# Optimization experiments

Measured on AMD Instinct MI355X. Metric: run time of the kernel, lower is better.

The kernel has to match this reference:

```python
import jax, jax.numpy as jnp
import numpy as np

N_NODES = 100000
BN_EPS = 1e-5


def gcn_conv(x, edge_index, W, b):
    # x: [N, Fin] -> [N, Fout]; symmetric-normalized aggregation with self-loops,
    # matching torch_geometric GCNConv defaults.
    n = x.shape[0]
    row, col = edge_index[0], edge_index[1]  # messages flow row -> col
    h = x @ W  # [N, Fout]
    deg = jnp.zeros((n,), dtype=h.dtype).at[col].add(1.0) + 1.0  # +1 for self-loop
    dinv = jax.lax.rsqrt(deg)  # deg >= 1 always
    norm = dinv[row] * dinv[col]  # [E]
    agg = jax.ops.segment_sum(h[row] * norm[:, None], col, num_segments=n)
    agg = agg + h * (dinv * dinv)[:, None]  # self-loop term, norm = 1/deg
    return agg + b


def batch_norm(x, gamma, beta):
    # BatchNorm1d in training mode: biased batch statistics over nodes.
    mean = jnp.mean(x, axis=0)
    var = jnp.mean((x - mean) ** 2, axis=0)
    return gamma * (x - mean) * jax.lax.rsqrt(var + BN_EPS) + beta


def setup_inputs() -> dict:
    key = jax.random.key(0)
    k = jax.random.split(key, 8)
    net_size1, hidden, net_size2 = 64, 128, 128
    x = jax.random.normal(k[0], (N_NODES, net_size1), dtype=jnp.float32)
    edge_index = jax.random.randint(k[1], (2, 1600000), 0, N_NODES, dtype=jnp.int64)
    s1 = 1.0 / np.sqrt(net_size1)
    s2 = 1.0 / np.sqrt(hidden)
    W1 = jax.random.normal(k[2], (net_size1, hidden), dtype=jnp.float32) * s1
    b1 = jnp.zeros((hidden,), dtype=jnp.float32)
    gamma = jnp.ones((hidden,), dtype=jnp.float32)
    beta = jnp.zeros((hidden,), dtype=jnp.float32)
    W2 = jax.random.normal(k[3], (hidden, net_size2), dtype=jnp.float32) * s2
    b2 = jnp.zeros((net_size2,), dtype=jnp.float32)
    return {"x": x, "edge_index": edge_index, "W1": W1, "b1": b1,
            "gamma": gamma, "beta": beta, "W2": W2, "b2": b2}


def reference(x, edge_index, W1, b1, gamma, beta, W2, b2):
    h = jax.nn.relu(gcn_conv(x, edge_index, W1, b1))
    h = batch_norm(h, gamma, beta)
    h = jax.nn.relu(gcn_conv(h, edge_index, W2, b2))
    return h
```

## Files before the change

kernel.cpp:

```cpp
#include <hip/hip_runtime.h>

#define BSZ_LG 9
#define BSZ 512

__device__ __forceinline__ float bf_lo(unsigned u) { return __uint_as_float(u << 16); }
__device__ __forceinline__ float bf_hi(unsigned u) { return __uint_as_float(u & 0xffff0000u); }
__device__ __forceinline__ float bf1(unsigned short s) { return __uint_as_float(((unsigned)s) << 16); }
__device__ __forceinline__ unsigned short f2bf(float f) {
    unsigned u = __float_as_uint(f);
    u += 0x7fffu + ((u >> 16) & 1u);
    return (unsigned short)(u >> 16);
}
__device__ __forceinline__ unsigned pack2(float a, float b) {
    return (unsigned)f2bf(a) | ((unsigned)f2bf(b) << 16);
}

__global__ void k_flags(const unsigned* __restrict__ x, const int* __restrict__ ei,
                        int* __restrict__ flagf, int* __restrict__ flage,
                        int* __restrict__ bcnt, int* __restrict__ stats) {
    int t = threadIdx.x;
    if (blockIdx.x == 0) {
        int c = 0;
        for (int i = t; i < 1024; i += 256) {
            unsigned e = (x[i] >> 23) & 0xffu;
            if (e >= 96u && e < 160u) c++;
        }
        __shared__ int s;
        if (t == 0) s = 0;
        __syncthreads();
        atomicAdd(&s, c);
        __syncthreads();
        if (t == 0) *flagf = (s > 512) ? 1 : 0;
    } else if (blockIdx.x == 1) {
        int nz = 0;
        for (int i = t; i < 2048; i += 256) nz |= ei[2 * i + 1];
        __shared__ int s2;
        if (t == 0) s2 = 0;
        __syncthreads();
        if (nz) atomicOr(&s2, 1);
        __syncthreads();
        if (t == 0) *flage = (s2 == 0) ? 1 : 0;
    } else if (blockIdx.x == 2) {
        bcnt[t] = 0;
    } else {
        stats[t] = 0;
    }
}

struct Cvt6 {
    const void* src[6];
    unsigned short* dst[6];
    int off[7];
};
__global__ void k_cvt6(Cvt6 a, const int* __restrict__ flagf) {
    int i = blockIdx.x * 256 + threadIdx.x;
    if (i >= a.off[6]) return;
    int s = 0;
#pragma unroll
    for (int j = 1; j < 6; ++j) if (i >= a.off[j]) s = j;
    int k = i - a.off[s];
    unsigned short v;
    if (*flagf) v = f2bf(((const float*)a.src[s])[k]);
    else        v = ((const unsigned short*)a.src[s])[k];
    a.dst[s][k] = v;
}

__global__ __launch_bounds__(256) void k_prep(
        const void* __restrict__ x, const float* __restrict__ dinv,
        const int* __restrict__ flagf, unsigned* __restrict__ xs32, int Nq) {
    int i = blockIdx.x * 256 + threadIdx.x;
    if (i >= Nq) return;
    int n = i >> 4;
    float di = dinv[n];
    float v0, v1, v2, v3;
    if (*flagf) {
        float4 f = ((const float4*)x)[i];
        v0 = f.x; v1 = f.y; v2 = f.z; v3 = f.w;
    } else {
        uint2 u = ((const uint2*)x)[i];
        v0 = bf_lo(u.x); v1 = bf_hi(u.x); v2 = bf_lo(u.y); v3 = bf_hi(u.y);
    }
    uint2 o; o.x = pack2(di * v0, di * v1); o.y = pack2(di * v2, di * v3);
    ((uint2*)xs32)[i] = o;
}

__global__ __launch_bounds__(256) void k_binA(
        const int* __restrict__ ei, const int* __restrict__ flage,
        int* __restrict__ bcnt, int E, int N, int NBUCK) {
    __shared__ int hist[256];
    int t = threadIdx.x;
    hist[t] = 0;
    __syncthreads();
    int st = *flage + 1;
    int base = blockIdx.x * 4096 + t;
#pragma unroll
    for (int i = 0; i < 16; ++i) {
        int e = base + i * 256;
        if (e < E) {
            int r = ei[(size_t)st * e];
            int c = ei[(size_t)st * (E + e)];
            if ((unsigned)r < (unsigned)N && (unsigned)c < (unsigned)N)
                atomicAdd(&hist[c >> BSZ_LG], 1);
        }
    }
    __syncthreads();
    if (t < NBUCK && hist[t] > 0) atomicAdd(&bcnt[t], hist[t]);
}

__global__ void k_bscan(const int* __restrict__ bcnt, int* __restrict__ bofs,
                        int* __restrict__ bcur, int NBUCK) {
    __shared__ int tmp[256];
    int t = threadIdx.x;
    int v = (t < NBUCK) ? bcnt[t] : 0;
    tmp[t] = v; __syncthreads();
    for (int off = 1; off < 256; off <<= 1) {
        int xv = (t >= off) ? tmp[t - off] : 0;
        __syncthreads();
        tmp[t] += xv;
        __syncthreads();
    }
    if (t < NBUCK) {
        int ex = tmp[t] - v;
        bofs[t] = ex;
        bcur[t] = ex;
        if (t == NBUCK - 1) bofs[NBUCK] = tmp[t];
    }
}

__global__ __launch_bounds__(256) void k_binB(
        const int* __restrict__ ei, const int* __restrict__ flage,
        int* __restrict__ bcur, unsigned* __restrict__ bins, int E, int N, int NBUCK) {
    __shared__ int hist[256], hincl[256], hofs[256], loc[256], gbase[256];
    __shared__ unsigned stage[4096];
    __shared__ unsigned char bseg[4096];
    int t = threadIdx.x;
    hist[t] = 0; loc[t] = 0;
    __syncthreads();
    int st = *flage + 1;
    int base = blockIdx.x * 4096 + t;
    int bs[16]; unsigned vs[16];
#pragma unroll
    for (int i = 0; i < 16; ++i) {
        int e = base + i * 256;
        bs[i] = -1; vs[i] = 0;
        if (e < E) {
            int r = ei[(size_t)st * e];
            int c = ei[(size_t)st * (E + e)];
            if ((unsigned)r < (unsigned)N && (unsigned)c < (unsigned)N) {
                bs[i] = c >> BSZ_LG;
                vs[i] = ((unsigned)r << BSZ_LG) | (unsigned)(c & (BSZ - 1));
                atomicAdd(&hist[bs[i]], 1);
            }
        }
    }
    __syncthreads();
    hincl[t] = hist[t];
    __syncthreads();
    for (int off = 1; off < 256; off <<= 1) {
        int xv = (t >= off) ? hincl[t - off] : 0;
        __syncthreads();
        hincl[t] += xv;
        __syncthreads();
    }
    hofs[t] = hincl[t] - hist[t];
    if (t < NBUCK && hist[t] > 0) gbase[t] = atomicAdd(&bcur[t], hist[t]);
    __syncthreads();
#pragma unroll
    for (int i = 0; i < 16; ++i) {
        if (bs[i] >= 0) {
            int l = atomicAdd(&loc[bs[i]], 1);
            int pos = hofs[bs[i]] + l;
            stage[pos] = vs[i];
            bseg[pos] = (unsigned char)bs[i];
        }
    }
    __syncthreads();
    int total = hincl[255];
    for (int j = t; j < total; j += 256) {
        int b = bseg[j];
        bins[gbase[b] + (j - hofs[b])] = stage[j];
    }
}

__global__ __launch_bounds__(512) void k_csr(
        const unsigned* __restrict__ bins, const int* __restrict__ bofs,
        int* __restrict__ csr, int* __restrict__ ofs, int* __restrict__ endv,
        float* __restrict__ dinv, int N) {
    __shared__ int tmp[BSZ];
    __shared__ int cur[BSZ];
    int b = blockIdx.x, t = threadIdx.x;
    int eb = bofs[b], ee = bofs[b + 1];
    tmp[t] = 0;
    __syncthreads();
    for (int p = eb + t; p < ee; p += BSZ)
        atomicAdd(&tmp[bins[p] & (BSZ - 1)], 1);
    __syncthreads();
    int v = tmp[t];
    for (int off = 1; off < BSZ; off <<= 1) {
        int xv = (t >= off) ? tmp[t - off] : 0;
        __syncthreads();
        tmp[t] += xv;
        __syncthreads();
    }
    int incl = tmp[t];
    int excl = incl - v;
    cur[t] = excl;
    int node = b * BSZ + t;
    if (node < N) {
        ofs[node]  = eb + excl;
        endv[node] = eb + incl;
        dinv[node] = rsqrtf((float)(v + 1));
    }
    __syncthreads();
    for (int p = eb + t; p < ee; p += BSZ) {
        unsigned x = bins[p];
        int cl = x & (BSZ - 1);
        int l = atomicAdd(&cur[cl], 1);
        csr[eb + l] = (int)(x >> BSZ_LG);
    }
}

__global__ __launch_bounds__(256) void k_agg1(
        const unsigned* __restrict__ xs32, const int* __restrict__ csr,
        const int* __restrict__ ofs, const int* __restrict__ endv,
        const float* __restrict__ dinv, unsigned* __restrict__ s1_32, int N) {
    int sub = threadIdx.x >> 5, lane = threadIdx.x & 31;
    int node = blockIdx.x * 8 + sub;
    if (node >= N) return;
    int beg = ofs[node], end = endv[node];
    unsigned self = xs32[(size_t)node * 32 + lane];
    float a0 = bf_lo(self), a1 = bf_hi(self);
    int p = beg;
    for (; p + 7 < end; p += 8) {
        int r0 = csr[p], r1 = csr[p+1], r2 = csr[p+2], r3 = csr[p+3];
        int r4 = csr[p+4], r5 = csr[p+5], r6 = csr[p+6], r7 = csr[p+7];
        unsigned u0 = xs32[(size_t)r0 * 32 + lane];
        unsigned u1 = xs32[(size_t)r1 * 32 + lane];
        unsigned u2 = xs32[(size_t)r2 * 32 + lane];
        unsigned u3 = xs32[(size_t)r3 * 32 + lane];
        unsigned u4 = xs32[(size_t)r4 * 32 + lane];
        unsigned u5 = xs32[(size_t)r5 * 32 + lane];
        unsigned u6 = xs32[(size_t)r6 * 32 + lane];
        unsigned u7 = xs32[(size_t)r7 * 32 + lane];
        a0 += bf_lo(u0) + bf_lo(u1) + bf_lo(u2) + bf_lo(u3)
            + bf_lo(u4) + bf_lo(u5) + bf_lo(u6) + bf_lo(u7);
        a1 += bf_hi(u0) + bf_hi(u1) + bf_hi(u2) + bf_hi(u3)
            + bf_hi(u4) + bf_hi(u5) + bf_hi(u6) + bf_hi(u7);
    }
    for (; p + 3 < end; p += 4) {
        int r0 = csr[p], r1 = csr[p+1], r2 = csr[p+2], r3 = csr[p+3];
        unsigned u0 = xs32[(size_t)r0 * 32 + lane];
        unsigned u1 = xs32[(size_t)r1 * 32 + lane];
        unsigned u2 = xs32[(size_t)r2 * 32 + lane];
        unsigned u3 = xs32[(size_t)r3 * 32 + lane];
        a0 += bf_lo(u0) + bf_lo(u1) + bf_lo(u2) + bf_lo(u3);
        a1 += bf_hi(u0) + bf_hi(u1) + bf_hi(u2) + bf_hi(u3);
    }
    for (; p < end; ++p) {
        unsigned u = xs32[(size_t)csr[p] * 32 + lane];
        a0 += bf_lo(u); a1 += bf_hi(u);
    }
    float di = dinv[node];
    s1_32[(size_t)node * 32 + lane] = pack2(di * a0, di * a1);
}

typedef __attribute__((ext_vector_type(8))) short bf16x8;
typedef __attribute__((ext_vector_type(4))) float f32x4;

template<int K, int OUTMODE>
__global__ __launch_bounds__(256) void k_mgemm(
        const unsigned short* __restrict__ A, const unsigned short* __restrict__ Wg,
        const unsigned short* __restrict__ bias, void* __restrict__ outv,
        const int* __restrict__ flagf, int N) {
    constexpr int KP = K + 8;
    __shared__ __align__(16) unsigned short sA[64 * KP];
    __shared__ __align__(16) unsigned short sW[128 * KP];
    int t = threadIdx.x;
    int n0 = blockIdx.x * 64;

    for (int i = t; i < K * 128; i += 256) {
        int k = i >> 7, n = i & 127;
        sW[n * KP + k] = Wg[i];
    }
    {
        constexpr int rowv = K / 8;
        const uint4* Av = (const uint4*)A;
        for (int i = t; i < 64 * rowv; i += 256) {
            int r = i / rowv, c = i % rowv;
            int node = n0 + r;
            uint4 v = make_uint4(0u, 0u, 0u, 0u);
            if (node < N) v = Av[(size_t)node * rowv + c];
            *(uint4*)&sA[r * KP + c * 8] = v;
        }
    }
    __syncthreads();

    int lane = t & 63, wave = t >> 6, quad = lane >> 4, l16 = lane & 15;
    int mb = wave * 16;

    f32x4 acc[8];
#pragma unroll
    for (int j = 0; j < 8; ++j) acc[j] = (f32x4){0.f, 0.f, 0.f, 0.f};

#pragma unroll
    for (int k0 = 0; k0 < K; k0 += 32) {
        bf16x8 af = *(const bf16x8*)&sA[(mb + l16) * KP + k0 + quad * 8];
#pragma unroll
        for (int tn = 0; tn < 8; ++tn) {
            bf16x8 bfv = *(const bf16x8*)&sW[(tn * 16 + l16) * KP + k0 + quad * 8];
            acc[tn] = __builtin_amdgcn_mfma_f32_16x16x32_bf16(af, bfv, acc[tn], 0, 0, 0);
        }
    }

    bool f32out = (OUTMODE == 1) && (*flagf != 0);
    int nodeb = n0 + mb + quad * 4;
#pragma unroll
    for (int tn = 0; tn < 8; ++tn) {
        float bv = bf1(bias[tn * 16 + l16]);
#pragma unroll
        for (int r = 0; r < 4; ++r) {
            int node = nodeb + r;
            if (node < N) {
                float v = fmaxf(acc[tn][r] + bv, 0.f);
                if (OUTMODE == 1 && f32out)
                    ((float*)outv)[(size_t)node * 128 + tn * 16 + l16] = v;
                else
                    ((unsigned short*)outv)[(size_t)node * 128 + tn * 16 + l16] = f2bf(v);
            }
        }
    }
}

__global__ __launch_bounds__(256) void k_bnstat(
        const unsigned short* __restrict__ h1, float* __restrict__ stats, int N) {
    __shared__ float sS[1024], sQ[1024];
    int t = threadIdx.x;
    int lane = t & 31, g = t >> 5;
    int f0 = lane * 4;
    float s0=0, s1=0, s2=0, s3=0, q0=0, q1=0, q2=0, q3=0;
    const uint2* h2 = (const uint2*)h1;
    for (int n = blockIdx.x * 8 + g; n < N; n += 2048) {
        uint2 u = h2[(size_t)n * 32 + lane];
        float v0 = bf_lo(u.x), v1 = bf_hi(u.x), v2 = bf_lo(u.y), v3 = bf_hi(u.y);
        s0 += v0; s1 += v1; s2 += v2; s3 += v3;
        q0 = fmaf(v0, v0, q0); q1 = fmaf(v1, v1, q1);
        q2 = fmaf(v2, v2, q2); q3 = fmaf(v3, v3, q3);
    }
    sS[g * 128 + f0 + 0] = s0; sS[g * 128 + f0 + 1] = s1;
    sS[g * 128 + f0 + 2] = s2; sS[g * 128 + f0 + 3] = s3;
    sQ[g * 128 + f0 + 0] = q0; sQ[g * 128 + f0 + 1] = q1;
    sQ[g * 128 + f0 + 2] = q2; sQ[g * 128 + f0 + 3] = q3;
    __syncthreads();
    if (t < 128) {
        float ss = 0, qq = 0;
#pragma unroll
        for (int gg = 0; gg < 8; ++gg) { ss += sS[gg * 128 + t]; qq += sQ[gg * 128 + t]; }
        atomicAdd(&stats[t], ss);
        atomicAdd(&stats[128 + t], qq);
    }
}

__global__ void k_bnfin(const float* __restrict__ stats,
                        const unsigned short* __restrict__ gamma,
                        const unsigned short* __restrict__ beta,
                        float* __restrict__ bnp, float invN) {
    int f = threadIdx.x;
    float mean = stats[f] * invN;
    float var = stats[128 + f] * invN - mean * mean;
    if (!(var >= 0.f)) var = 0.f;
    float sc = bf1(gamma[f]) * rsqrtf(var + 1e-5f);
    bnp[f] = sc;
    bnp[128 + f] = bf1(beta[f]) - mean * sc;
}

__global__ __launch_bounds__(256) void k_bnapply(
        const unsigned short* __restrict__ h1, const float* __restrict__ bnp,
        const float* __restrict__ dinv, unsigned short* __restrict__ gb, int N) {
    int idx = blockIdx.x * 256 + threadIdx.x;
    if (idx >= N * 16) return;
    int n = idx >> 4;
    int f0 = (idx & 15) * 8;
    float di = dinv[n];
    uint4 h = *(const uint4*)&h1[(size_t)n * 128 + f0];
    float v0 = di * (bnp[f0 + 0] * bf_lo(h.x) + bnp[128 + f0 + 0]);
    float v1 = di * (bnp[f0 + 1] * bf_hi(h.x) + bnp[128 + f0 + 1]);
    float v2 = di * (bnp[f0 + 2] * bf_lo(h.y) + bnp[128 + f0 + 2]);
    float v3 = di * (bnp[f0 + 3] * bf_hi(h.y) + bnp[128 + f0 + 3]);
    float v4 = di * (bnp[f0 + 4] * bf_lo(h.z) + bnp[128 + f0 + 4]);
    float v5 = di * (bnp[f0 + 5] * bf_hi(h.z) + bnp[128 + f0 + 5]);
    float v6 = di * (bnp[f0 + 6] * bf_lo(h.w) + bnp[128 + f0 + 6]);
    float v7 = di * (bnp[f0 + 7] * bf_hi(h.w) + bnp[128 + f0 + 7]);
    uint4 o;
    o.x = pack2(v0, v1); o.y = pack2(v2, v3);
    o.z = pack2(v4, v5); o.w = pack2(v6, v7);
    *(uint4*)&gb[(size_t)n * 128 + f0] = o;
}

__global__ __launch_bounds__(256) void k_agg2(
        const unsigned short* __restrict__ gb, const int* __restrict__ csr,
        const int* __restrict__ ofs, const int* __restrict__ endv,
        const float* __restrict__ dinv, unsigned short* __restrict__ s2, int N) {
    int sub = threadIdx.x >> 5, lane = threadIdx.x & 31;
    int node = blockIdx.x * 8 + sub;
    if (node >= N) return;
    const uint2* g2 = (const uint2*)gb;
    int beg = ofs[node], end = endv[node];
    uint2 self = g2[(size_t)node * 32 + lane];
    float a0 = bf_lo(self.x), a1 = bf_hi(self.x), a2 = bf_lo(self.y), a3 = bf_hi(self.y);
    int p = beg;
    for (; p + 7 < end; p += 8) {
        int r0 = csr[p], r1 = csr[p+1], r2 = csr[p+2], r3 = csr[p+3];
        int r4 = csr[p+4], r5 = csr[p+5], r6 = csr[p+6], r7 = csr[p+7];
        uint2 u0 = g2[(size_t)r0 * 32 + lane];
        uint2 u1 = g2[(size_t)r1 * 32 + lane];
        uint2 u2 = g2[(size_t)r2 * 32 + lane];
        uint2 u3 = g2[(size_t)r3 * 32 + lane];
        uint2 u4 = g2[(size_t)r4 * 32 + lane];
        uint2 u5 = g2[(size_t)r5 * 32 + lane];
        uint2 u6 = g2[(size_t)r6 * 32 + lane];
        uint2 u7 = g2[(size_t)r7 * 32 + lane];
        a0 += bf_lo(u0.x) + bf_lo(u1.x) + bf_lo(u2.x) + bf_lo(u3.x)
            + bf_lo(u4.x) + bf_lo(u5.x) + bf_lo(u6.x) + bf_lo(u7.x);
        a1 += bf_hi(u0.x) + bf_hi(u1.x) + bf_hi(u2.x) + bf_hi(u3.x)
            + bf_hi(u4.x) + bf_hi(u5.x) + bf_hi(u6.x) + bf_hi(u7.x);
        a2 += bf_lo(u0.y) + bf_lo(u1.y) + bf_lo(u2.y) + bf_lo(u3.y)
            + bf_lo(u4.y) + bf_lo(u5.y) + bf_lo(u6.y) + bf_lo(u7.y);
        a3 += bf_hi(u0.y) + bf_hi(u1.y) + bf_hi(u2.y) + bf_hi(u3.y)
            + bf_hi(u4.y) + bf_hi(u5.y) + bf_hi(u6.y) + bf_hi(u7.y);
    }
    for (; p + 3 < end; p += 4) {
        int r0 = csr[p], r1 = csr[p+1], r2 = csr[p+2], r3 = csr[p+3];
        uint2 u0 = g2[(size_t)r0 * 32 + lane];
        uint2 u1 = g2[(size_t)r1 * 32 + lane];
        uint2 u2 = g2[(size_t)r2 * 32 + lane];
        uint2 u3 = g2[(size_t)r3 * 32 + lane];
        a0 += bf_lo(u0.x) + bf_lo(u1.x) + bf_lo(u2.x) + bf_lo(u3.x);
        a1 += bf_hi(u0.x) + bf_hi(u1.x) + bf_hi(u2.x) + bf_hi(u3.x);
        a2 += bf_lo(u0.y) + bf_lo(u1.y) + bf_lo(u2.y) + bf_lo(u3.y);
        a3 += bf_hi(u0.y) + bf_hi(u1.y) + bf_hi(u2.y) + bf_hi(u3.y);
    }
    for (; p < end; ++p) {
        uint2 u = g2[(size_t)csr[p] * 32 + lane];
        a0 += bf_lo(u.x); a1 += bf_hi(u.x); a2 += bf_lo(u.y); a3 += bf_hi(u.y);
    }
    float di = dinv[node];
    uint2 o; o.x = pack2(di * a0, di * a1); o.y = pack2(di * a2, di * a3);
    ((uint2*)s2)[(size_t)node * 32 + lane] = o;
}

extern "C" void kernel_launch(void* const* d_in, const int* in_sizes, int n_in,
                              void* d_out, int out_size, void* d_ws, size_t ws_size,
                              hipStream_t stream) {
    const int N = in_sizes[0] / 64;
    const int E = in_sizes[1] / 2;
    const int nW1 = in_sizes[2], nb1 = in_sizes[3], ngm = in_sizes[4],
              nbt = in_sizes[5], nW2 = in_sizes[6], nb2 = in_sizes[7];
    const int NBUCK = (N + BSZ - 1) >> BSZ_LG;

    const int* ei = (const int*)d_in[1];

    char* w = (char*)d_ws;
    size_t off = 0;
    auto alloc = [&](size_t bytes) -> void* {
        void* p = w + off;
        off = (off + bytes + 255) & ~(size_t)255;
        return p;
    };
    int*   bcnt   = (int*)alloc(256 * 4);
    int*   bofs   = (int*)alloc(257 * 4);
    int*   bcur   = (int*)alloc(256 * 4);
    int*   flagf  = (int*)alloc(256);
    int*   flage  = (int*)alloc(256);
    int*   ofs    = (int*)alloc((size_t)N * 4);
    int*   endv   = (int*)alloc((size_t)N * 4);
    int*   csr    = (int*)alloc((size_t)E * 4);
    float* dinv   = (float*)alloc((size_t)N * 4);
    float* stats  = (float*)alloc(512 * 4);
    unsigned* xs32 = (unsigned*)alloc((size_t)N * 64 * 2);
    unsigned short* wb = (unsigned short*)alloc((size_t)32768 * 2);
    char* reg1 = (char*)alloc((size_t)N * 64 * 4);
    char* reg2 = (char*)alloc((size_t)N * 128 * 2);
    unsigned* bins = (unsigned*)reg1;
    unsigned short* s1 = (unsigned short*)reg1;
    unsigned short* gb = (unsigned short*)reg1;
    unsigned short* h1 = (unsigned short*)reg2;
    unsigned short* s2 = (unsigned short*)reg2;

    unsigned short* W1b = wb;
    unsigned short* b1b = W1b + nW1;
    unsigned short* gmb = b1b + nb1;
    unsigned short* btb = gmb + ngm;
    unsigned short* W2b = btb + nbt;
    unsigned short* b2b = W2b + nW2;

    const int NCH = (E + 4095) / 4096;

    k_flags <<<4, 256, 0, stream>>>((const unsigned*)d_in[0], ei, flagf, flage,
                                    bcnt, (int*)stats);
    Cvt6 ca;
    ca.src[0] = d_in[2]; ca.dst[0] = W1b;
    ca.src[1] = d_in[3]; ca.dst[1] = b1b;
    ca.src[2] = d_in[4]; ca.dst[2] = gmb;
    ca.src[3] = d_in[5]; ca.dst[3] = btb;
    ca.src[4] = d_in[6]; ca.dst[4] = W2b;
    ca.src[5] = d_in[7]; ca.dst[5] = b2b;
    int szs[6] = {nW1, nb1, ngm, nbt, nW2, nb2};
    ca.off[0] = 0;
    for (int i = 0; i < 6; ++i) ca.off[i + 1] = ca.off[i] + szs[i];
    k_cvt6 <<<(ca.off[6] + 255) / 256, 256, 0, stream>>>(ca, flagf);

    k_binA  <<<NCH, 256, 0, stream>>>(ei, flage, bcnt, E, N, NBUCK);
    k_bscan <<<1, 256, 0, stream>>>(bcnt, bofs, bcur, NBUCK);
    k_binB  <<<NCH, 256, 0, stream>>>(ei, flage, bcur, bins, E, N, NBUCK);
    k_csr   <<<NBUCK, BSZ, 0, stream>>>(bins, bofs, csr, ofs, endv, dinv, N);

    k_prep  <<<(N * 16 + 255) / 256, 256, 0, stream>>>(d_in[0], dinv, flagf, xs32, N * 16);
    k_agg1  <<<(N + 7) / 8, 256, 0, stream>>>(xs32, csr, ofs, endv, dinv, (unsigned*)s1, N);
    k_mgemm<64, 0><<<(N + 63) / 64, 256, 0, stream>>>(s1, W1b, b1b, h1, flagf, N);
    k_bnstat<<<256, 256, 0, stream>>>(h1, stats, N);
    k_bnfin <<<1, 128, 0, stream>>>(stats, gmb, btb, stats + 256, 1.0f / (float)N);
    k_bnapply<<<((size_t)N * 16 + 255) / 256, 256, 0, stream>>>(h1, stats + 256, dinv, gb, N);
    k_agg2  <<<(N + 7) / 8, 256, 0, stream>>>(gb, csr, ofs, endv, dinv, s2, N);
    k_mgemm<128, 1><<<(N + 63) / 64, 256, 0, stream>>>(s2, W2b, b2b, d_out, flagf, N);
}
```

Baseline: 315.4 us.

## Fuse prep into CSR build, merge BN finalize into apply, widen gathers

Folds the input scaling pass into the CSR kernel, since each bucket block already knows its nodes' degrees. BN finalize is recomputed per block inside the apply kernel. The end-offset array is replaced by a single N+1 offset array. Aggregation 1 now uses 16 lanes per node with 8-byte loads, and both aggregations gather 16 neighbours per unrolled step. Together these remove two launches and some memory traffic and add more loads in flight, at the cost of extra register pressure and redundant BN parameter work in every block.

```diff
diff --git a/kernel.cpp b/kernel.cpp
--- a/kernel.cpp
+++ b/kernel.cpp
@@ -63,25 +63,6 @@
     if (*flagf) v = f2bf(((const float*)a.src[s])[k]);
     else        v = ((const unsigned short*)a.src[s])[k];
     a.dst[s][k] = v;
-}
-
-__global__ __launch_bounds__(256) void k_prep(
-        const void* __restrict__ x, const float* __restrict__ dinv,
-        const int* __restrict__ flagf, unsigned* __restrict__ xs32, int Nq) {
-    int i = blockIdx.x * 256 + threadIdx.x;
-    if (i >= Nq) return;
-    int n = i >> 4;
-    float di = dinv[n];
-    float v0, v1, v2, v3;
-    if (*flagf) {
-        float4 f = ((const float4*)x)[i];
-        v0 = f.x; v1 = f.y; v2 = f.z; v3 = f.w;
-    } else {
-        uint2 u = ((const uint2*)x)[i];
-        v0 = bf_lo(u.x); v1 = bf_hi(u.x); v2 = bf_lo(u.y); v3 = bf_hi(u.y);
-    }
-    uint2 o; o.x = pack2(di * v0, di * v1); o.y = pack2(di * v2, di * v3);
-    ((uint2*)xs32)[i] = o;
 }
 
 __global__ __launch_bounds__(256) void k_binA(
@@ -184,10 +165,12 @@
 
 __global__ __launch_bounds__(512) void k_csr(
         const unsigned* __restrict__ bins, const int* __restrict__ bofs,
-        int* __restrict__ csr, int* __restrict__ ofs, int* __restrict__ endv,
-        float* __restrict__ dinv, int N) {
+        const void* __restrict__ x, const int* __restrict__ flagf,
+        int* __restrict__ csr, int* __restrict__ ofs,
+        float* __restrict__ dinv, unsigned* __restrict__ xs32, int N) {
     __shared__ int tmp[BSZ];
     __shared__ int cur[BSZ];
+    __shared__ float sdi[BSZ];
     int b = blockIdx.x, t = threadIdx.x;
     int eb = bofs[b], ee = bofs[b + 1];
     tmp[t] = 0;
@@ -205,63 +188,99 @@
     int incl = tmp[t];
     int excl = incl - v;
     cur[t] = excl;
+    float di = rsqrtf((float)(v + 1));
+    sdi[t] = di;
     int node = b * BSZ + t;
     if (node < N) {
         ofs[node]  = eb + excl;
-        endv[node] = eb + incl;
-        dinv[node] = rsqrtf((float)(v + 1));
+        dinv[node] = di;
+        if (node == N - 1) ofs[N] = eb + incl;
     }
     __syncthreads();
     for (int p = eb + t; p < ee; p += BSZ) {
-        unsigned x = bins[p];
-        int cl = x & (BSZ - 1);
+        unsigned xx = bins[p];
+        int cl = xx & (BSZ - 1);
         int l = atomicAdd(&cur[cl], 1);
-        csr[eb + l] = (int)(x >> BSZ_LG);
+        csr[eb + l] = (int)(xx >> BSZ_LG);
+    }
+    bool f32 = (*flagf != 0);
+    int nbase = b * BSZ;
+    for (int i = t; i < BSZ * 16; i += BSZ) {
+        int nl = i >> 4;
+        int n = nbase + nl;
+        if (n >= N) break;
+        float d2 = sdi[nl];
+        float v0, v1, v2, v3;
+        if (f32) {
+            float4 f = ((const float4*)x)[(size_t)n * 16 + (i & 15)];
+            v0 = f.x; v1 = f.y; v2 = f.z; v3 = f.w;
+        } else {
+            uint2 u = ((const uint2*)x)[(size_t)n * 16 + (i & 15)];
+            v0 = bf_lo(u.x); v1 = bf_hi(u.x); v2 = bf_lo(u.y); v3 = bf_hi(u.y);
+        }
+        uint2 o; o.x = pack2(d2 * v0, d2 * v1); o.y = pack2(d2 * v2, d2 * v3);
+        ((uint2*)xs32)[(size_t)n * 16 + (i & 15)] = o;
     }
 }
 
 __global__ __launch_bounds__(256) void k_agg1(
         const unsigned* __restrict__ xs32, const int* __restrict__ csr,
-        const int* __restrict__ ofs, const int* __restrict__ endv,
-        const float* __restrict__ dinv, unsigned* __restrict__ s1_32, int N) {
-    int sub = threadIdx.x >> 5, lane = threadIdx.x & 31;
-    int node = blockIdx.x * 8 + sub;
+        const int* __restrict__ ofs, const float* __restrict__ dinv,
+        unsigned* __restrict__ s1_32, int N) {
+    int lane = threadIdx.x & 15, sub = threadIdx.x >> 4;
+    int node = blockIdx.x * 16 + sub;
     if (node >= N) return;
-    int beg = ofs[node], end = endv[node];
-    unsigned self = xs32[(size_t)node * 32 + lane];
-    float a0 = bf_lo(self), a1 = bf_hi(self);
+    const uint2* x2 = (const uint2*)xs32;
+    int beg = ofs[node], end = ofs[node + 1];
+    uint2 self = x2[(size_t)node * 16 + lane];
+    float a0 = bf_lo(self.x), a1 = bf_hi(self.x), a2 = bf_lo(self.y), a3 = bf_hi(self.y);
     int p = beg;
-    for (; p + 7 < end; p += 8) {
-        int r0 = csr[p], r1 = csr[p+1], r2 = csr[p+2], r3 = csr[p+3];
-        int r4 = csr[p+4], r5 = csr[p+5], r6 = csr[p+6], r7 = csr[p+7];
-        unsigned u0 = xs32[(size_t)r0 * 32 + lane];
-        unsigned u1 = xs32[(size_t)r1 * 32 + lane];
-        unsigned u2 = xs32[(size_t)r2 * 32 + lane];
-        unsigned u3 = xs32[(size_t)r3 * 32 + lane];
-        unsigned u4 = xs32[(size_t)r4 * 32 + lane];
-        unsigned u5 = xs32[(size_t)r5 * 32 + lane];
-        unsigned u6 = xs32[(size_t)r6 * 32 + lane];
-        unsigned u7 = xs32[(size_t)r7 * 32 + lane];
-        a0 += bf_lo(u0) + bf_lo(u1) + bf_lo(u2) + bf_lo(u3)
-            + bf_lo(u4) + bf_lo(u5) + bf_lo(u6) + bf_lo(u7);
-        a1 += bf_hi(u0) + bf_hi(u1) + bf_hi(u2) + bf_hi(u3)
-            + bf_hi(u4) + bf_hi(u5) + bf_hi(u6) + bf_hi(u7);
-    }
-    for (; p + 3 < end; p += 4) {
-        int r0 = csr[p], r1 = csr[p+1], r2 = csr[p+2], r3 = csr[p+3];
-        unsigned u0 = xs32[(size_t)r0 * 32 + lane];
-        unsigned u1 = xs32[(size_t)r1 * 32 + lane];
-        unsigned u2 = xs32[(size_t)r2 * 32 + lane];
-        unsigned u3 = xs32[(size_t)r3 * 32 + lane];
-        a0 += bf_lo(u0) + bf_lo(u1) + bf_lo(u2) + bf_lo(u3);
-        a1 += bf_hi(u0) + bf_hi(u1) + bf_hi(u2) + bf_hi(u3);
+    while (p + 15 < end) {
+        int r[16]; uint2 u[16];
+#pragma unroll
+        for (int j = 0; j < 16; ++j) r[j] = csr[p + j];
+#pragma unroll
+        for (int j = 0; j < 16; ++j) u[j] = x2[(size_t)r[j] * 16 + lane];
+#pragma unroll
+        for (int j = 0; j < 16; ++j) {
+            a0 += bf_lo(u[j].x); a1 += bf_hi(u[j].x);
+            a2 += bf_lo(u[j].y); a3 += bf_hi(u[j].y);
+        }
+        p += 16;
+    }
+    if (p + 7 < end) {
+        int r[8]; uint2 u[8];
+#pragma unroll
+        for (int j = 0; j < 8; ++j) r[j] = csr[p + j];
+#pragma unroll
+        for (int j = 0; j < 8; ++j) u[j] = x2[(size_t)r[j] * 16 + lane];
+#pragma unroll
+        for (int j = 0; j < 8; ++j) {
+            a0 += bf_lo(u[j].x); a1 += bf_hi(u[j].x);
+            a2 += bf_lo(u[j].y); a3 += bf_hi(u[j].y);
+        }
+        p += 8;
+    }
+    if (p + 3 < end) {
+        int r[4]; uint2 u[4];
+#pragma unroll
+        for (int j = 0; j < 4; ++j) r[j] = csr[p + j];
+#pragma unroll
+        for (int j = 0; j < 4; ++j) u[j] = x2[(size_t)r[j] * 16 + lane];
+#pragma unroll
+        for (int j = 0; j < 4; ++j) {
+            a0 += bf_lo(u[j].x); a1 += bf_hi(u[j].x);
+            a2 += bf_lo(u[j].y); a3 += bf_hi(u[j].y);
+        }
+        p += 4;
     }
     for (; p < end; ++p) {
-        unsigned u = xs32[(size_t)csr[p] * 32 + lane];
-        a0 += bf_lo(u); a1 += bf_hi(u);
+        uint2 u = x2[(size_t)csr[p] * 16 + lane];
+        a0 += bf_lo(u.x); a1 += bf_hi(u.x); a2 += bf_lo(u.y); a3 += bf_hi(u.y);
     }
     float di = dinv[node];
-    s1_32[(size_t)node * 32 + lane] = pack2(di * a0, di * a1);
+    uint2 o; o.x = pack2(di * a0, di * a1); o.y = pack2(di * a2, di * a3);
+    ((uint2*)s1_32)[(size_t)node * 16 + lane] = o;
 }
 
 typedef __attribute__((ext_vector_type(8))) short bf16x8;
@@ -360,36 +379,36 @@
     }
 }
 
-__global__ void k_bnfin(const float* __restrict__ stats,
-                        const unsigned short* __restrict__ gamma,
-                        const unsigned short* __restrict__ beta,
-                        float* __restrict__ bnp, float invN) {
-    int f = threadIdx.x;
-    float mean = stats[f] * invN;
-    float var = stats[128 + f] * invN - mean * mean;
-    if (!(var >= 0.f)) var = 0.f;
-    float sc = bf1(gamma[f]) * rsqrtf(var + 1e-5f);
-    bnp[f] = sc;
-    bnp[128 + f] = bf1(beta[f]) - mean * sc;
-}
-
 __global__ __launch_bounds__(256) void k_bnapply(
-        const unsigned short* __restrict__ h1, const float* __restrict__ bnp,
-        const float* __restrict__ dinv, unsigned short* __restrict__ gb, int N) {
-    int idx = blockIdx.x * 256 + threadIdx.x;
+        const unsigned short* __restrict__ h1, const float* __restrict__ stats,
+        const unsigned short* __restrict__ gamma, const unsigned short* __restrict__ beta,
+        const float* __restrict__ dinv, unsigned short* __restrict__ gb,
+        float invN, int N) {
+    __shared__ float sp[256];
+    int t = threadIdx.x;
+    if (t < 128) {
+        float mean = stats[t] * invN;
+        float var = stats[128 + t] * invN - mean * mean;
+        if (!(var >= 0.f)) var = 0.f;
+        float sc = bf1(gamma[t]) * rsqrtf(var + 1e-5f);
+        sp[t] = sc;
+        sp[128 + t] = bf1(beta[t]) - mean * sc;
+    }
+    __syncthreads();
+    int idx = blockIdx.x * 256 + t;
     if (idx >= N * 16) return;
     int n = idx >> 4;
     int f0 = (idx & 15) * 8;
     float di = dinv[n];
     uint4 h = *(const uint4*)&h1[(size_t)n * 128 + f0];
-    float v0 = di * (bnp[f0 + 0] * bf_lo(h.x) + bnp[128 + f0 + 0]);
-    float v1 = di * (bnp[f0 + 1] * bf_hi(h.x) + bnp[128 + f0 + 1]);
-    float v2 = di * (bnp[f0 + 2] * bf_lo(h.y) + bnp[128 + f0 + 2]);
-    float v3 = di * (bnp[f0 + 3] * bf_hi(h.y) + bnp[128 + f0 + 3]);
-    float v4 = di * (bnp[f0 + 4] * bf_lo(h.z) + bnp[128 + f0 + 4]);
-    float v5 = di * (bnp[f0 + 5] * bf_hi(h.z) + bnp[128 + f0 + 5]);
-    float v6 = di * (bnp[f0 + 6] * bf_lo(h.w) + bnp[128 + f0 + 6]);
-    float v7 = di * (bnp[f0 + 7] * bf_hi(h.w) + bnp[128 + f0 + 7]);
+    float v0 = di * (sp[f0 + 0] * bf_lo(h.x) + sp[128 + f0 + 0]);
+    float v1 = di * (sp[f0 + 1] * bf_hi(h.x) + sp[128 + f0 + 1]);
+    float v2 = di * (sp[f0 + 2] * bf_lo(h.y) + sp[128 + f0 + 2]);
+    float v3 = di * (sp[f0 + 3] * bf_hi(h.y) + sp[128 + f0 + 3]);
+    float v4 = di * (sp[f0 + 4] * bf_lo(h.z) + sp[128 + f0 + 4]);
+    float v5 = di * (sp[f0 + 5] * bf_hi(h.z) + sp[128 + f0 + 5]);
+    float v6 = di * (sp[f0 + 6] * bf_lo(h.w) + sp[128 + f0 + 6]);
+    float v7 = di * (sp[f0 + 7] * bf_hi(h.w) + sp[128 + f0 + 7]);
     uint4 o;
     o.x = pack2(v0, v1); o.y = pack2(v2, v3);
     o.z = pack2(v4, v5); o.w = pack2(v6, v7);
@@ -398,46 +417,54 @@
 
 __global__ __launch_bounds__(256) void k_agg2(
         const unsigned short* __restrict__ gb, const int* __restrict__ csr,
-        const int* __restrict__ ofs, const int* __restrict__ endv,
-        const float* __restrict__ dinv, unsigned short* __restrict__ s2, int N) {
+        const int* __restrict__ ofs, const float* __restrict__ dinv,
+        unsigned short* __restrict__ s2, int N) {
     int sub = threadIdx.x >> 5, lane = threadIdx.x & 31;
     int node = blockIdx.x * 8 + sub;
     if (node >= N) return;
     const uint2* g2 = (const uint2*)gb;
-    int beg = ofs[node], end = endv[node];
+    int beg = ofs[node], end = ofs[node + 1];
     uint2 self = g2[(size_t)node * 32 + lane];
     float a0 = bf_lo(self.x), a1 = bf_hi(self.x), a2 = bf_lo(self.y), a3 = bf_hi(self.y);
     int p = beg;
-    for (; p + 7 < end; p += 8) {
-        int r0 = csr[p], r1 = csr[p+1], r2 = csr[p+2], r3 = csr[p+3];
-        int r4 = csr[p+4], r5 = csr[p+5], r6 = csr[p+6], r7 = csr[p+7];
-        uint2 u0 = g2[(size_t)r0 * 32 + lane];
-        uint2 u1 = g2[(size_t)r1 * 32 + lane];
-        uint2 u2 = g2[(size_t)r2 * 32 + lane];
-        uint2 u3 = g2[(size_t)r3 * 32 + lane];
-        uint2 u4 = g2[(size_t)r4 * 32 + lane];
-        uint2 u5 = g2[(size_t)r5 * 32 + lane];
-        uint2 u6 = g2[(size_t)r6 * 32 + lane];
-        uint2 u7 = g2[(size_t)r7 * 32 + lane];
-        a0 += bf_lo(u0.x) + bf_lo(u1.x) + bf_lo(u2.x) + bf_lo(u3.x)
-            + bf_lo(u4.x) + bf_lo(u5.x) + bf_lo(u6.x) + bf_lo(u7.x);
-        a1 += bf_hi(u0.x) + bf_hi(u1.x) + bf_hi(u2.x) + bf_hi(u3.x)
-            + bf_hi(u4.x) + bf_hi(u5.x) + bf_hi(u6.x) + bf_hi(u7.x);
-        a2 += bf_lo(u0.y) + bf_lo(u1.y) + bf_lo(u2.y) + bf_lo(u3.y)
-            + bf_lo(u4.y) + bf_lo(u5.y) + bf_lo(u6.y) + bf_lo(u7.y);
-        a3 += bf_hi(u0.y) + bf_hi(u1.y) + bf_hi(u2.y) + bf_hi(u3.y)
-            + bf_hi(u4.y) + bf_hi(u5.y) + bf_hi(u6.y) + bf_hi(u7.y);
-    }
-    for (; p + 3 < end; p += 4) {
-        int r0 = csr[p], r1 = csr[p+1], r2 = csr[p+2], r3 = csr[p+3];
-        uint2 u0 = g2[(size_t)r0 * 32 + lane];
-        uint2 u1 = g2[(size_t)r1 * 32 + lane];
-        uint2 u2 = g2[(size_t)r2 * 32 + lane];
-        uint2 u3 = g2[(size_t)r3 * 32 + lane];
-        a0 += bf_lo(u0.x) + bf_lo(u1.x) + bf_lo(u2.x) + bf_lo(u3.x);
-        a1 += bf_hi(u0.x) + bf_hi(u1.x) + bf_hi(u2.x) + bf_hi(u3.x);
-        a2 += bf_lo(u0.y) + bf_lo(u1.y) + bf_lo(u2.y) + bf_lo(u3.y);
-        a3 += bf_hi(u0.y) + bf_hi(u1.y) + bf_hi(u2.y) + bf_hi(u3.y);
+    while (p + 15 < end) {
+        int r[16]; uint2 u[16];
+#pragma unroll
+        for (int j = 0; j < 16; ++j) r[j] = csr[p + j];
+#pragma unroll
+        for (int j = 0; j < 16; ++j) u[j] = g2[(size_t)r[j] * 32 + lane];
+#pragma unroll
+        for (int j = 0; j < 16; ++j) {
+            a0 += bf_lo(u[j].x); a1 += bf_hi(u[j].x);
+            a2 += bf_lo(u[j].y); a3 += bf_hi(u[j].y);
+        }
+        p += 16;
+    }
+    if (p + 7 < end) {
+        int r[8]; uint2 u[8];
+#pragma unroll
+        for (int j = 0; j < 8; ++j) r[j] = csr[p + j];
+#pragma unroll
+        for (int j = 0; j < 8; ++j) u[j] = g2[(size_t)r[j] * 32 + lane];
+#pragma unroll
+        for (int j = 0; j < 8; ++j) {
+            a0 += bf_lo(u[j].x); a1 += bf_hi(u[j].x);
+            a2 += bf_lo(u[j].y); a3 += bf_hi(u[j].y);
+        }
+        p += 8;
+    }
+    if (p + 3 < end) {
+        int r[4]; uint2 u[4];
+#pragma unroll
+        for (int j = 0; j < 4; ++j) r[j] = csr[p + j];
+#pragma unroll
+        for (int j = 0; j < 4; ++j) u[j] = g2[(size_t)r[j] * 32 + lane];
+#pragma unroll
+        for (int j = 0; j < 4; ++j) {
+            a0 += bf_lo(u[j].x); a1 += bf_hi(u[j].x);
+            a2 += bf_lo(u[j].y); a3 += bf_hi(u[j].y);
+        }
+        p += 4;
     }
     for (; p < end; ++p) {
         uint2 u = g2[(size_t)csr[p] * 32 + lane];
@@ -471,8 +498,7 @@
     int*   bcur   = (int*)alloc(256 * 4);
     int*   flagf  = (int*)alloc(256);
     int*   flage  = (int*)alloc(256);
-    int*   ofs    = (int*)alloc((size_t)N * 4);
-    int*   endv   = (int*)alloc((size_t)N * 4);
+    int*   ofs    = (int*)alloc(((size_t)N + 1) * 4);
     int*   csr    = (int*)alloc((size_t)E * 4);
     float* dinv   = (float*)alloc((size_t)N * 4);
     float* stats  = (float*)alloc(512 * 4);
@@ -512,14 +538,14 @@
     k_binA  <<<NCH, 256, 0, stream>>>(ei, flage, bcnt, E, N, NBUCK);
     k_bscan <<<1, 256, 0, stream>>>(bcnt, bofs, bcur, NBUCK);
     k_binB  <<<NCH, 256, 0, stream>>>(ei, flage, bcur, bins, E, N, NBUCK);
-    k_csr   <<<NBUCK, BSZ, 0, stream>>>(bins, bofs, csr, ofs, endv, dinv, N);
-
-    k_prep  <<<(N * 16 + 255) / 256, 256, 0, stream>>>(d_in[0], dinv, flagf, xs32, N * 16);
-    k_agg1  <<<(N + 7) / 8, 256, 0, stream>>>(xs32, csr, ofs, endv, dinv, (unsigned*)s1, N);
+    k_csr   <<<NBUCK, BSZ, 0, stream>>>(bins, bofs, d_in[0], flagf,
+                                        csr, ofs, dinv, xs32, N);
+
+    k_agg1  <<<(N + 15) / 16, 256, 0, stream>>>(xs32, csr, ofs, dinv, (unsigned*)s1, N);
     k_mgemm<64, 0><<<(N + 63) / 64, 256, 0, stream>>>(s1, W1b, b1b, h1, flagf, N);
     k_bnstat<<<256, 256, 0, stream>>>(h1, stats, N);
-    k_bnfin <<<1, 128, 0, stream>>>(stats, gmb, btb, stats + 256, 1.0f / (float)N);
-    k_bnapply<<<((size_t)N * 16 + 255) / 256, 256, 0, stream>>>(h1, stats + 256, dinv, gb, N);
-    k_agg2  <<<(N + 7) / 8, 256, 0, stream>>>(gb, csr, ofs, endv, dinv, s2, N);
+    k_bnapply<<<((size_t)N * 16 + 255) / 256, 256, 0, stream>>>(
+        h1, stats, gmb, btb, dinv, gb, 1.0f / (float)N, N);
+    k_agg2  <<<(N + 7) / 8, 256, 0, stream>>>(gb, csr, ofs, dinv, s2, N);
     k_mgemm<128, 1><<<(N + 63) / 64, 256, 0, stream>>>(s2, W2b, b2b, d_out, flagf, N);
 }
```

Result: slower. 326.7 us (+3.6%).
